# Kernel tuning notes

Measured on AMD Instinct MI355X. Metric: run time of the kernel, lower is better.

The kernel has to match this reference:

```python
import jax, jax.numpy as jnp
import numpy as np

N1 = 100000  # source cloud size (x1)
N2 = 100000  # target cloud size (x2)
F = 64       # point feature dim
E = 1600000  # number of radius edges (avg 16 neighbors)
H = 128      # MLP hidden/out dim


def setup_inputs() -> dict:
    key = jax.random.key(0)
    ks = jax.random.split(key, 12)
    s = 0.05
    return {
        "x1_features": jax.random.normal(ks[0], (N1, F), jnp.float32),
        "x1_pos": jax.random.normal(ks[1], (N1, 3), jnp.float32),
        "x2_features": jax.random.normal(ks[2], (N2, F), jnp.float32),
        "x2_pos": jax.random.normal(ks[3], (N2, 3), jnp.float32),
        "W1": jax.random.normal(ks[4], (2 * F + 3, H), jnp.float32) * s,
        "b1": jnp.zeros((H,), jnp.float32),
        "W2": jax.random.normal(ks[5], (H, H), jnp.float32) * s,
        "b2": jnp.zeros((H,), jnp.float32),
        "W3": jax.random.normal(ks[6], (H, H), jnp.float32) * s,
        "b3": jnp.zeros((H,), jnp.float32),
        "edge_src": jax.random.randint(ks[7], (E,), 0, N1, jnp.int32),
        "edge_dst": jax.random.randint(ks[8], (E,), 0, N2, jnp.int32),
    }


def reference(x1_features, x1_pos, x2_features, x2_pos,
              W1, b1, W2, b2, W3, b3, edge_src, edge_dst):
    # message(x_i, x_j, pos_i, pos_j): i = target (x2, edge_dst), j = source (x1, edge_src)
    # msg = cat([x_i, x_j, pos_j - pos_i], dim=1)  -> [E, 2F+3]
    msg = jnp.concatenate(
        [x2_features[edge_dst],
         x1_features[edge_src],
         x1_pos[edge_src] - x2_pos[edge_dst]], axis=1)
    # MLP (Linear+ReLU x3, FastFlow3D make_mlp style)
    h = jax.nn.relu(msg @ W1 + b1)
    h = jax.nn.relu(h @ W2 + b2)
    h = jax.nn.relu(h @ W3 + b3)
    # scatter-max aggregation onto x2 nodes; PyG fills empty segments with 0
    out = jax.ops.segment_max(h, edge_dst, num_segments=N2)
    out = jnp.where(jnp.isneginf(out), 0.0, out)
    return out, x2_pos
```

## Files before the change

### kernel.cpp

```cpp
#include <hip/hip_runtime.h>
#include <hip/hip_bf16.h>

#define DEV __device__ __forceinline__

typedef short bf16x8 __attribute__((ext_vector_type(8)));
typedef float f32x16 __attribute__((ext_vector_type(16)));

static constexpr int FDIM  = 64;
static constexpr int HH    = 128;
static constexpr int KPAD  = 144;
static constexpr int KS    = KPAD / 16;
static constexpr int TM    = 256;

static constexpr int CSTR  = TM * 16 + 256 + 16;
static constexpr int HBUF  = 16 * CSTR;
static constexpr int L_TOT = HBUF + TM * 4;

static constexpr int WTL      = KPAD * HH;
static constexpr int WT_TOTAL = 3 * WTL;

DEV unsigned pack2(float a, float b) {
    union { __hip_bfloat162 h; unsigned u; } cv;
    cv.h.x = __float2bfloat16(a);
    cv.h.y = __float2bfloat16(b);
    return cv.u;
}
DEV unsigned short f2bf(float f) {
    union { __hip_bfloat16 h; unsigned short u; } cv;
    cv.h = __float2bfloat16(f);
    return cv.u;
}
DEV int rowoff(int r) { return r * 16 + (r >> 3) * 8; }

__global__ void k_cvt(const float* __restrict__ src, unsigned short* __restrict__ dst, int n8) {
    int i = blockIdx.x * 256 + threadIdx.x;
    if (i < n8) {
        float4 a = *(const float4*)(src + (size_t)i * 8);
        float4 b = *(const float4*)(src + (size_t)i * 8 + 4);
        uint4 o;
        o.x = pack2(a.x, a.y); o.y = pack2(a.z, a.w);
        o.z = pack2(b.x, b.y); o.w = pack2(b.z, b.w);
        *(uint4*)(dst + (size_t)i * 8) = o;
    }
}

__global__ void k_wprep(const float* __restrict__ W1, const float* __restrict__ b1,
                        const float* __restrict__ W2, const float* __restrict__ b2,
                        const float* __restrict__ W3, const float* __restrict__ b3,
                        unsigned short* __restrict__ wt) {
    int i = blockIdx.x * 256 + threadIdx.x;
    if (i >= WT_TOTAL) return;
    int layer = i / WTL, j = i % WTL;
    int n = j / KPAD, k = j % KPAD;
    float v = 0.f;
    if (layer == 0) {
        if (k < 131) v = W1[k * HH + n];
        else if (k == 131) v = b1[n];
    } else {
        const float* W = (layer == 1) ? W2 : W3;
        const float* b = (layer == 1) ? b2 : b3;
        if (k < 128) v = W[k * HH + n];
        else if (k == 128) v = b[n];
    }
    wt[i] = f2bf(v);
}

__global__ void k_hist(const int* __restrict__ edst, int* __restrict__ cnt, int E) {
    int e = blockIdx.x * 256 + threadIdx.x;
    if (e < E) atomicAdd(&cnt[edst[e]], 1);
}

__global__ void k_scan_part(const int* __restrict__ cnt, int* __restrict__ partial, int n2) {
    __shared__ int sm[256];
    int t = threadIdx.x;
    int base = blockIdx.x * 1024 + t * 4;
    int s = 0;
#pragma unroll
    for (int j = 0; j < 4; j++) { int idx = base + j; if (idx < n2) s += cnt[idx]; }
    sm[t] = s; __syncthreads();
    for (int off = 128; off > 0; off >>= 1) {
        if (t < off) sm[t] += sm[t + off];
        __syncthreads();
    }
    if (t == 0) partial[blockIdx.x] = sm[0];
}

__global__ void k_scan_top(int* __restrict__ partial, int nb) {
    __shared__ int sm[256];
    int t = threadIdx.x;
    int v = (t < nb) ? partial[t] : 0;
    sm[t] = v; __syncthreads();
    for (int off = 1; off < 256; off <<= 1) {
        int add = (t >= off) ? sm[t - off] : 0;
        __syncthreads();
        sm[t] += add;
        __syncthreads();
    }
    if (t < nb) partial[t] = sm[t] - v;
}

__global__ void k_scan_down(const int* __restrict__ cnt, const int* __restrict__ partial,
                            int* __restrict__ cursor, int n2) {
    __shared__ int sm[256];
    int t = threadIdx.x;
    int base = blockIdx.x * 1024 + t * 4;
    int c[4]; int s = 0;
#pragma unroll
    for (int j = 0; j < 4; j++) { int idx = base + j; c[j] = (idx < n2) ? cnt[idx] : 0; s += c[j]; }
    sm[t] = s; __syncthreads();
    for (int off = 1; off < 256; off <<= 1) {
        int add = (t >= off) ? sm[t - off] : 0;
        __syncthreads();
        sm[t] += add;
        __syncthreads();
    }
    int run = partial[blockIdx.x] + (sm[t] - s);
#pragma unroll
    for (int j = 0; j < 4; j++) {
        int idx = base + j;
        if (idx < n2) cursor[idx] = run;
        run += c[j];
    }
}

__global__ void k_fill(const int* __restrict__ edst, const int* __restrict__ esrc,
                       int* __restrict__ cursor,
                       int* __restrict__ csr_s, int* __restrict__ csr_d, int E) {
    int e = blockIdx.x * 256 + threadIdx.x;
    if (e < E) {
        int d = edst[e];
        int p = atomicAdd(&cursor[d], 1);
        csr_s[p] = esrc[e];
        csr_d[p] = d;
    }
}

DEV f32x16 zerov() {
    f32x16 v;
#pragma unroll
    for (int i = 0; i < 16; i++) v[i] = 0.f;
    return v;
}
DEV float relu(float x) { return fmaxf(x, 0.f); }

DEV void layer_reg(const unsigned short* __restrict__ wtl, const unsigned pkin[32],
                   unsigned pkout[32], int l31, int hh, unsigned biasw) {
    unsigned xv[16];
#pragma unroll
    for (int ks = 0; ks < 8; ks++) {
        unsigned t0 = hh ? pkin[4 * ks + 0] : pkin[4 * ks + 2];
        unsigned t1 = hh ? pkin[4 * ks + 1] : pkin[4 * ks + 3];
        xv[2 * ks + 0] = (unsigned)__shfl_xor((int)t0, 32, 64);
        xv[2 * ks + 1] = (unsigned)__shfl_xor((int)t1, 32, 64);
    }
#pragma unroll
    for (int rt = 0; rt < 4; rt++) {
        f32x16 acc = zerov();
#pragma unroll
        for (int ks = 0; ks < 8; ks++) {
            union { unsigned u[4]; bf16x8 v; } B;
            B.u[0] = hh ? xv[2 * ks + 0]   : pkin[4 * ks + 0];
            B.u[1] = hh ? xv[2 * ks + 1]   : pkin[4 * ks + 1];
            B.u[2] = hh ? pkin[4 * ks + 2] : xv[2 * ks + 0];
            B.u[3] = hh ? pkin[4 * ks + 3] : xv[2 * ks + 1];
            bf16x8 A = *(const bf16x8*)(wtl + (rt * 32 + l31) * KPAD + ks * 16 + 8 * hh);
            acc = __builtin_amdgcn_mfma_f32_32x32x16_bf16(A, B.v, acc, 0, 0, 0);
        }
        {
            union { unsigned u[4]; bf16x8 v; } B;
            B.u[0] = biasw; B.u[1] = 0u; B.u[2] = 0u; B.u[3] = 0u;
            bf16x8 A = *(const bf16x8*)(wtl + (rt * 32 + l31) * KPAD + 8 * 16 + 8 * hh);
            acc = __builtin_amdgcn_mfma_f32_32x32x16_bf16(A, B.v, acc, 0, 0, 0);
        }
#pragma unroll
        for (int g = 0; g < 4; g++) {
            pkout[8 * rt + 2 * g + 0] = pack2(relu(acc[4 * g + 0]), relu(acc[4 * g + 1]));
            pkout[8 * rt + 2 * g + 1] = pack2(relu(acc[4 * g + 2]), relu(acc[4 * g + 3]));
        }
    }
}

template <bool SORTED, bool BF16SRC>
__global__ __launch_bounds__(512, 4) void k_main(
    const float* __restrict__ x1f, const float* __restrict__ x1p,
    const float* __restrict__ x2f, const float* __restrict__ x2p,
    const char* __restrict__ xb1, const char* __restrict__ xb2,
    const unsigned short* __restrict__ wt,
    const int* __restrict__ csr_s, const int* __restrict__ csr_d,
    const int* __restrict__ edge_src, const int* __restrict__ edge_dst,
    float* __restrict__ out, int E) {
    __shared__ __align__(16) char smem[L_TOT];
    char* hbf = smem;
    int*  dl  = (int*)(smem + HBUF);

    const int tid  = threadIdx.x;
    const int lane = tid & 63;
    const int wv   = tid >> 6;
    const int l31  = lane & 31;
    const int hh   = lane >> 5;
    const int eb   = blockIdx.x * TM;
    const int r    = wv * 32 + l31;
    const int slot = eb + r;
    const bool ok  = slot < E;

    int d = 0, s = 0;
    if (ok) {
        d = SORTED ? csr_d[slot] : edge_dst[slot];
        s = SORTED ? csr_s[slot] : edge_src[slot];
    }
    if (hh == 0) dl[r] = ok ? d : -1;

    bf16x8 Bv[KS];
    if (BF16SRC) {
        const char* bx2 = xb2 + (size_t)d * (2 * FDIM);
        const char* bx1 = xb1 + (size_t)s * (2 * FDIM);
#pragma unroll
        for (int ks = 0; ks < 4; ks++)
            Bv[ks] = *(const bf16x8*)(bx2 + (2 * ks + hh) * 16);
#pragma unroll
        for (int ks = 4; ks < 8; ks++)
            Bv[ks] = *(const bf16x8*)(bx1 + (2 * (ks - 4) + hh) * 16);
    } else {
        const float* fx2 = x2f + (size_t)d * FDIM;
        const float* fx1 = x1f + (size_t)s * FDIM;
#pragma unroll
        for (int ks = 0; ks < 8; ks++) {
            const float* b = (ks < 4) ? (fx2 + (2 * ks + hh) * 8)
                                      : (fx1 + (2 * (ks - 4) + hh) * 8);
            float4 a0 = *(const float4*)(b);
            float4 a1 = *(const float4*)(b + 4);
            union { unsigned u[4]; bf16x8 v; } B;
            B.u[0] = pack2(a0.x, a0.y); B.u[1] = pack2(a0.z, a0.w);
            B.u[2] = pack2(a1.x, a1.y); B.u[3] = pack2(a1.z, a1.w);
            Bv[ks] = B.v;
        }
    }
    {
        float dx = 0.f, dy = 0.f, dz = 0.f;
        if (ok) {
            dx = x1p[s * 3 + 0] - x2p[d * 3 + 0];
            dy = x1p[s * 3 + 1] - x2p[d * 3 + 1];
            dz = x1p[s * 3 + 2] - x2p[d * 3 + 2];
        }
        union { unsigned u[4]; bf16x8 v; } P;
        P.u[0] = hh ? 0u : pack2(dx, dy);
        P.u[1] = hh ? 0u : pack2(dz, 1.0f);
        P.u[2] = 0u; P.u[3] = 0u;
        Bv[8] = P.v;
    }

    unsigned pkA[32], pkB[32];
#pragma unroll
    for (int rt = 0; rt < 4; rt++) {
        f32x16 acc = zerov();
#pragma unroll
        for (int ks = 0; ks < KS; ks++) {
            bf16x8 A = *(const bf16x8*)(wt + (rt * 32 + l31) * KPAD + ks * 16 + 8 * hh);
            acc = __builtin_amdgcn_mfma_f32_32x32x16_bf16(A, Bv[ks], acc, 0, 0, 0);
        }
#pragma unroll
        for (int g = 0; g < 4; g++) {
            pkA[8 * rt + 2 * g + 0] = pack2(relu(acc[4 * g + 0]), relu(acc[4 * g + 1]));
            pkA[8 * rt + 2 * g + 1] = pack2(relu(acc[4 * g + 2]), relu(acc[4 * g + 3]));
        }
    }

    const unsigned biasw = hh ? 0u : 0x00003F80u;
    layer_reg(wt + WTL,     pkA, pkB, l31, hh, biasw);
    layer_reg(wt + 2 * WTL, pkB, pkA, l31, hh, biasw);

    {
        char* dst = hbf + rowoff(r) + 8 * hh;
#pragma unroll
        for (int u = 0; u < 16; u++) {
            uint2 w; w.x = pkA[2 * u + 0]; w.y = pkA[2 * u + 1];
            *(uint2*)(dst + u * CSTR) = w;
        }
    }
    __syncthreads();

    {
        const int p     = tid & 63;
        const int strip = tid >> 6;
        const int r0 = strip * 32;
        const char* fbase = hbf + (p >> 2) * CSTR + (p & 3) * 4;
        int curd = dl[r0];
        int rs = r0;
        float m0 = 0.f, m1 = 0.f;
#pragma unroll 4
        for (int rr = r0; rr < r0 + 32; rr++) {
            int dd = dl[rr];
            if (dd != curd) {
                if (curd >= 0) {
                    bool extL = (rs == r0) && (r0 == 0 || dl[r0 - 1] == curd);
                    if (extL) {
                        if (m0 > 0.f) atomicMax((int*)out + (size_t)curd * HH + 2 * p,     __float_as_int(m0));
                        if (m1 > 0.f) atomicMax((int*)out + (size_t)curd * HH + 2 * p + 1, __float_as_int(m1));
                    } else {
                        out[(size_t)curd * HH + 2 * p]     = m0;
                        out[(size_t)curd * HH + 2 * p + 1] = m1;
                    }
                }
                curd = dd; rs = rr; m0 = 0.f; m1 = 0.f;
            }
            unsigned w = *(const unsigned*)(fbase + rowoff(rr));
            m0 = fmaxf(m0, __uint_as_float(w << 16));
            m1 = fmaxf(m1, __uint_as_float(w & 0xffff0000u));
        }
        if (curd >= 0) {
            bool extL = (rs == r0) && (r0 == 0 || dl[r0 - 1] == curd);
            bool extR = (r0 + 32 == TM) || (dl[r0 + 32] == curd);
            if (extL || extR) {
                if (m0 > 0.f) atomicMax((int*)out + (size_t)curd * HH + 2 * p,     __float_as_int(m0));
                if (m1 > 0.f) atomicMax((int*)out + (size_t)curd * HH + 2 * p + 1, __float_as_int(m1));
            } else {
                out[(size_t)curd * HH + 2 * p]     = m0;
                out[(size_t)curd * HH + 2 * p + 1] = m1;
            }
        }
    }
}

extern "C" void kernel_launch(void* const* d_in, const int* in_sizes, int n_in,
                              void* d_out, int out_size, void* d_ws, size_t ws_size,
                              hipStream_t stream) {
    const float* x1f = (const float*)d_in[0];
    const float* x1p = (const float*)d_in[1];
    const float* x2f = (const float*)d_in[2];
    const float* x2p = (const float*)d_in[3];
    const float* W1  = (const float*)d_in[4];
    const float* b1  = (const float*)d_in[5];
    const float* W2  = (const float*)d_in[6];
    const float* b2  = (const float*)d_in[7];
    const float* W3  = (const float*)d_in[8];
    const float* b3  = (const float*)d_in[9];
    const int* esrc  = (const int*)d_in[10];
    const int* edst  = (const int*)d_in[11];
    const int E  = in_sizes[10];
    const int N1 = in_sizes[1] / 3;
    const int N2 = in_sizes[3] / 3;
    float* out = (float*)d_out;

    size_t off = 0;
    auto take = [&](size_t bytes) { size_t o = off; off = (off + bytes + 255) & ~(size_t)255; return o; };
    size_t o_cnt = take(4 * (size_t)N2);
    size_t o_cur = take(4 * (size_t)N2);
    size_t o_par = take(4 * 256);
    size_t o_cs  = take(4 * (size_t)E);
    size_t o_cd  = take(4 * (size_t)E);
    size_t o_wt  = take(2 * (size_t)WT_TOTAL);
    size_t need_csr = off;
    size_t o_x1  = take(2 * (size_t)N1 * FDIM);
    size_t o_x2  = take(2 * (size_t)N2 * FDIM);
    size_t need_bf = off;

    const int NB = (N2 + 1023) / 1024;
    bool use_csr = (need_csr <= ws_size) && (NB <= 256);
    bool use_bf  = (need_bf <= ws_size);

    char* ws = (char*)d_ws;
    unsigned short* wt = use_csr ? (unsigned short*)(ws + o_wt) : (unsigned short*)ws;
    int* cnt    = (int*)(ws + o_cnt);
    int* cursor = (int*)(ws + o_cur);
    int* part   = (int*)(ws + o_par);
    int* csr_s  = (int*)(ws + o_cs);
    int* csr_d  = (int*)(ws + o_cd);
    char* xb1   = ws + o_x1;
    char* xb2   = ws + o_x2;

    (void)hipMemsetAsync(out, 0, (size_t)N2 * HH * 4, stream);
    (void)hipMemcpyAsync(out + (size_t)N2 * HH, x2p, (size_t)N2 * 3 * 4,
                         hipMemcpyDeviceToDevice, stream);

    k_wprep<<<(WT_TOTAL + 255) / 256, 256, 0, stream>>>(W1, b1, W2, b2, W3, b3, wt);

    if (use_bf) {
        int n8_1 = N1 * FDIM / 8, n8_2 = N2 * FDIM / 8;
        k_cvt<<<(n8_1 + 255) / 256, 256, 0, stream>>>(x1f, (unsigned short*)xb1, n8_1);
        k_cvt<<<(n8_2 + 255) / 256, 256, 0, stream>>>(x2f, (unsigned short*)xb2, n8_2);
    }

    const int grid = (E + TM - 1) / TM;
    if (use_csr) {
        (void)hipMemsetAsync(cnt, 0, 4 * (size_t)N2, stream);
        k_hist<<<(E + 255) / 256, 256, 0, stream>>>(edst, cnt, E);
        k_scan_part<<<NB, 256, 0, stream>>>(cnt, part, N2);
        k_scan_top<<<1, 256, 0, stream>>>(part, NB);
        k_scan_down<<<NB, 256, 0, stream>>>(cnt, part, cursor, N2);
        k_fill<<<(E + 255) / 256, 256, 0, stream>>>(edst, esrc, cursor, csr_s, csr_d, E);
        if (use_bf)
            k_main<true, true><<<grid, 512, 0, stream>>>(
                x1f, x1p, x2f, x2p, xb1, xb2, wt, csr_s, csr_d, esrc, edst, out, E);
        else
            k_main<true, false><<<grid, 512, 0, stream>>>(
                x1f, x1p, x2f, x2p, xb1, xb2, wt, csr_s, csr_d, esrc, edst, out, E);
    } else {
        if (use_bf)
            k_main<false, true><<<grid, 512, 0, stream>>>(
                x1f, x1p, x2f, x2p, xb1, xb2, wt, edst, edst, esrc, edst, out, E);
        else
            k_main<false, false><<<grid, 512, 0, stream>>>(
                x1f, x1p, x2f, x2p, xb1, xb2, wt, edst, edst, esrc, edst, out, E);
    }
}
```

Measured before the change: 616.0 us.

## Stage MLP weights in LDS and do segment-max with wave shuffles

All three layers' bf16 weights are re-laid out into per-k-step chunks and copied into a 108KB shared-memory buffer at block start, so MFMA A-operands come from LDS instead of global/L2. The LDS-staged scatter-max is replaced by a segmented shuffle-up scan over each 32-edge half-wave using packed bf16 max, with only segment tails issuing atomicMax. Blocks grow to 1024 threads covering 512 edges. This trades the per-block weight copy and large LDS footprint, which limits blocks per CU, and 32 edge boundaries instead of 256 mean more atomics.

```diff
diff --git a/kernel.cpp b/kernel.cpp
--- a/kernel.cpp
+++ b/kernel.cpp
@@ -5,19 +5,15 @@
 
 typedef short bf16x8 __attribute__((ext_vector_type(8)));
 typedef float f32x16 __attribute__((ext_vector_type(16)));
-
-static constexpr int FDIM  = 64;
-static constexpr int HH    = 128;
-static constexpr int KPAD  = 144;
-static constexpr int KS    = KPAD / 16;
-static constexpr int TM    = 256;
-
-static constexpr int CSTR  = TM * 16 + 256 + 16;
-static constexpr int HBUF  = 16 * CSTR;
-static constexpr int L_TOT = HBUF + TM * 4;
-
-static constexpr int WTL      = KPAD * HH;
-static constexpr int WT_TOTAL = 3 * WTL;
+typedef unsigned short u16x2 __attribute__((ext_vector_type(2)));
+
+static constexpr int FDIM = 64;
+static constexpr int HH   = 128;
+static constexpr int TM   = 512;
+static constexpr int CH   = 4096;
+static constexpr int NCH  = 27;
+static constexpr int WB   = NCH * CH;
+static constexpr int WT_ELEMS = NCH * 2048;
 
 DEV unsigned pack2(float a, float b) {
     union { __hip_bfloat162 h; unsigned u; } cv;
@@ -30,7 +26,11 @@
     cv.h = __float2bfloat16(f);
     return cv.u;
 }
-DEV int rowoff(int r) { return r * 16 + (r >> 3) * 8; }
+DEV unsigned pmax2(unsigned a, unsigned b) {
+    u16x2 av = __builtin_bit_cast(u16x2, a);
+    u16x2 bv = __builtin_bit_cast(u16x2, b);
+    return __builtin_bit_cast(unsigned, __builtin_elementwise_max(av, bv));
+}
 
 __global__ void k_cvt(const float* __restrict__ src, unsigned short* __restrict__ dst, int n8) {
     int i = blockIdx.x * 256 + threadIdx.x;
@@ -49,9 +49,11 @@
                         const float* __restrict__ W3, const float* __restrict__ b3,
                         unsigned short* __restrict__ wt) {
     int i = blockIdx.x * 256 + threadIdx.x;
-    if (i >= WT_TOTAL) return;
-    int layer = i / WTL, j = i % WTL;
-    int n = j / KPAD, k = j % KPAD;
+    if (i >= WT_ELEMS) return;
+    int c = i >> 11, r = i & 2047;
+    int n = r >> 4, half = (r >> 3) & 1, e = r & 7;
+    int layer = c / 9, ks = c % 9;
+    int k = ks * 16 + half * 8 + e;
     float v = 0.f;
     if (layer == 0) {
         if (k < 131) v = W1[k * HH + n];
@@ -143,7 +145,7 @@
 }
 DEV float relu(float x) { return fmaxf(x, 0.f); }
 
-DEV void layer_reg(const unsigned short* __restrict__ wtl, const unsigned pkin[32],
+DEV void layer_reg(const char* __restrict__ wl, const unsigned pkin[32],
                    unsigned pkout[32], int l31, int hh, unsigned biasw) {
     unsigned xv[16];
 #pragma unroll
@@ -155,6 +157,7 @@
     }
 #pragma unroll
     for (int rt = 0; rt < 4; rt++) {
+        const char* arow = wl + (rt * 32 + l31) * 32 + hh * 16;
         f32x16 acc = zerov();
 #pragma unroll
         for (int ks = 0; ks < 8; ks++) {
@@ -163,13 +166,13 @@
             B.u[1] = hh ? xv[2 * ks + 1]   : pkin[4 * ks + 1];
             B.u[2] = hh ? pkin[4 * ks + 2] : xv[2 * ks + 0];
             B.u[3] = hh ? pkin[4 * ks + 3] : xv[2 * ks + 1];
-            bf16x8 A = *(const bf16x8*)(wtl + (rt * 32 + l31) * KPAD + ks * 16 + 8 * hh);
+            bf16x8 A = *(const bf16x8*)(arow + ks * CH);
             acc = __builtin_amdgcn_mfma_f32_32x32x16_bf16(A, B.v, acc, 0, 0, 0);
         }
         {
             union { unsigned u[4]; bf16x8 v; } B;
             B.u[0] = biasw; B.u[1] = 0u; B.u[2] = 0u; B.u[3] = 0u;
-            bf16x8 A = *(const bf16x8*)(wtl + (rt * 32 + l31) * KPAD + 8 * 16 + 8 * hh);
+            bf16x8 A = *(const bf16x8*)(arow + 8 * CH);
             acc = __builtin_amdgcn_mfma_f32_32x32x16_bf16(A, B.v, acc, 0, 0, 0);
         }
 #pragma unroll
@@ -181,7 +184,7 @@
 }
 
 template <bool SORTED, bool BF16SRC>
-__global__ __launch_bounds__(512, 4) void k_main(
+__global__ __launch_bounds__(1024, 4) void k_main(
     const float* __restrict__ x1f, const float* __restrict__ x1p,
     const float* __restrict__ x2f, const float* __restrict__ x2p,
     const char* __restrict__ xb1, const char* __restrict__ xb2,
@@ -189,9 +192,7 @@
     const int* __restrict__ csr_s, const int* __restrict__ csr_d,
     const int* __restrict__ edge_src, const int* __restrict__ edge_dst,
     float* __restrict__ out, int E) {
-    __shared__ __align__(16) char smem[L_TOT];
-    char* hbf = smem;
-    int*  dl  = (int*)(smem + HBUF);
+    __shared__ __align__(16) char wlds[WB];
 
     const int tid  = threadIdx.x;
     const int lane = tid & 63;
@@ -199,21 +200,31 @@
     const int l31  = lane & 31;
     const int hh   = lane >> 5;
     const int eb   = blockIdx.x * TM;
+
+    {
+        const uint4* src = (const uint4*)wt;
+        uint4* dst = (uint4*)wlds;
+#pragma unroll
+        for (int j = tid; j < WB / 16; j += 1024)
+            dst[j] = src[j];
+    }
+    __syncthreads();
+
     const int r    = wv * 32 + l31;
     const int slot = eb + r;
     const bool ok  = slot < E;
-
-    int d = 0, s = 0;
+    int d = -1, s = 0;
     if (ok) {
         d = SORTED ? csr_d[slot] : edge_dst[slot];
         s = SORTED ? csr_s[slot] : edge_src[slot];
     }
-    if (hh == 0) dl[r] = ok ? d : -1;
-
-    bf16x8 Bv[KS];
+    const int dg = (d < 0) ? 0 : d;
+    const int sg = s;
+
+    bf16x8 Bv[9];
     if (BF16SRC) {
-        const char* bx2 = xb2 + (size_t)d * (2 * FDIM);
-        const char* bx1 = xb1 + (size_t)s * (2 * FDIM);
+        const char* bx2 = xb2 + (size_t)dg * (2 * FDIM);
+        const char* bx1 = xb1 + (size_t)sg * (2 * FDIM);
 #pragma unroll
         for (int ks = 0; ks < 4; ks++)
             Bv[ks] = *(const bf16x8*)(bx2 + (2 * ks + hh) * 16);
@@ -221,8 +232,8 @@
         for (int ks = 4; ks < 8; ks++)
             Bv[ks] = *(const bf16x8*)(bx1 + (2 * (ks - 4) + hh) * 16);
     } else {
-        const float* fx2 = x2f + (size_t)d * FDIM;
-        const float* fx1 = x1f + (size_t)s * FDIM;
+        const float* fx2 = x2f + (size_t)dg * FDIM;
+        const float* fx1 = x1f + (size_t)sg * FDIM;
 #pragma unroll
         for (int ks = 0; ks < 8; ks++) {
             const float* b = (ks < 4) ? (fx2 + (2 * ks + hh) * 8)
@@ -238,9 +249,9 @@
     {
         float dx = 0.f, dy = 0.f, dz = 0.f;
         if (ok) {
-            dx = x1p[s * 3 + 0] - x2p[d * 3 + 0];
-            dy = x1p[s * 3 + 1] - x2p[d * 3 + 1];
-            dz = x1p[s * 3 + 2] - x2p[d * 3 + 2];
+            dx = x1p[sg * 3 + 0] - x2p[dg * 3 + 0];
+            dy = x1p[sg * 3 + 1] - x2p[dg * 3 + 1];
+            dz = x1p[sg * 3 + 2] - x2p[dg * 3 + 2];
         }
         union { unsigned u[4]; bf16x8 v; } P;
         P.u[0] = hh ? 0u : pack2(dx, dy);
@@ -252,10 +263,11 @@
     unsigned pkA[32], pkB[32];
 #pragma unroll
     for (int rt = 0; rt < 4; rt++) {
+        const char* arow = wlds + (rt * 32 + l31) * 32 + hh * 16;
         f32x16 acc = zerov();
 #pragma unroll
-        for (int ks = 0; ks < KS; ks++) {
-            bf16x8 A = *(const bf16x8*)(wt + (rt * 32 + l31) * KPAD + ks * 16 + 8 * hh);
+        for (int ks = 0; ks < 9; ks++) {
+            bf16x8 A = *(const bf16x8*)(arow + ks * CH);
             acc = __builtin_amdgcn_mfma_f32_32x32x16_bf16(A, Bv[ks], acc, 0, 0, 0);
         }
 #pragma unroll
@@ -266,57 +278,32 @@
     }
 
     const unsigned biasw = hh ? 0u : 0x00003F80u;
-    layer_reg(wt + WTL,     pkA, pkB, l31, hh, biasw);
-    layer_reg(wt + 2 * WTL, pkB, pkA, l31, hh, biasw);
-
-    {
-        char* dst = hbf + rowoff(r) + 8 * hh;
-#pragma unroll
-        for (int u = 0; u < 16; u++) {
-            uint2 w; w.x = pkA[2 * u + 0]; w.y = pkA[2 * u + 1];
-            *(uint2*)(dst + u * CSTR) = w;
-        }
-    }
-    __syncthreads();
-
-    {
-        const int p     = tid & 63;
-        const int strip = tid >> 6;
-        const int r0 = strip * 32;
-        const char* fbase = hbf + (p >> 2) * CSTR + (p & 3) * 4;
-        int curd = dl[r0];
-        int rs = r0;
-        float m0 = 0.f, m1 = 0.f;
-#pragma unroll 4
-        for (int rr = r0; rr < r0 + 32; rr++) {
-            int dd = dl[rr];
-            if (dd != curd) {
-                if (curd >= 0) {
-                    bool extL = (rs == r0) && (r0 == 0 || dl[r0 - 1] == curd);
-                    if (extL) {
-                        if (m0 > 0.f) atomicMax((int*)out + (size_t)curd * HH + 2 * p,     __float_as_int(m0));
-                        if (m1 > 0.f) atomicMax((int*)out + (size_t)curd * HH + 2 * p + 1, __float_as_int(m1));
-                    } else {
-                        out[(size_t)curd * HH + 2 * p]     = m0;
-                        out[(size_t)curd * HH + 2 * p + 1] = m1;
-                    }
-                }
-                curd = dd; rs = rr; m0 = 0.f; m1 = 0.f;
-            }
-            unsigned w = *(const unsigned*)(fbase + rowoff(rr));
-            m0 = fmaxf(m0, __uint_as_float(w << 16));
-            m1 = fmaxf(m1, __uint_as_float(w & 0xffff0000u));
-        }
-        if (curd >= 0) {
-            bool extL = (rs == r0) && (r0 == 0 || dl[r0 - 1] == curd);
-            bool extR = (r0 + 32 == TM) || (dl[r0 + 32] == curd);
-            if (extL || extR) {
-                if (m0 > 0.f) atomicMax((int*)out + (size_t)curd * HH + 2 * p,     __float_as_int(m0));
-                if (m1 > 0.f) atomicMax((int*)out + (size_t)curd * HH + 2 * p + 1, __float_as_int(m1));
-            } else {
-                out[(size_t)curd * HH + 2 * p]     = m0;
-                out[(size_t)curd * HH + 2 * p + 1] = m1;
-            }
+    layer_reg(wlds + 9 * CH,  pkA, pkB, l31, hh, biasw);
+    layer_reg(wlds + 18 * CH, pkB, pkA, l31, hh, biasw);
+
+    const int dn = __shfl_down(d, 1, 32);
+#pragma unroll
+    for (int off = 1; off < 32; off <<= 1) {
+        int nd = __shfl_up(d, off, 32);
+        bool take = (l31 >= off) && (nd == d);
+#pragma unroll
+        for (int u = 0; u < 32; u++) {
+            unsigned nv = (unsigned)__shfl_up((int)pkA[u], off, 32);
+            unsigned mx = pmax2(pkA[u], nv);
+            pkA[u] = take ? mx : pkA[u];
+        }
+    }
+    const bool flush = (d >= 0) && ((l31 == 31) || (dn != d));
+    if (flush) {
+        int* op = (int*)out + (size_t)d * HH;
+#pragma unroll
+        for (int u = 0; u < 32; u++) {
+            const int feat = 32 * (u >> 3) + 8 * ((u >> 1) & 3) + 4 * hh + 2 * (u & 1);
+            unsigned w = pkA[u];
+            float lo = __uint_as_float(w << 16);
+            float hi = __uint_as_float(w & 0xffff0000u);
+            if (lo > 0.f) atomicMax(op + feat,     __float_as_int(lo));
+            if (hi > 0.f) atomicMax(op + feat + 1, __float_as_int(hi));
         }
     }
 }
@@ -348,7 +335,7 @@
     size_t o_par = take(4 * 256);
     size_t o_cs  = take(4 * (size_t)E);
     size_t o_cd  = take(4 * (size_t)E);
-    size_t o_wt  = take(2 * (size_t)WT_TOTAL);
+    size_t o_wt  = take(2 * (size_t)WT_ELEMS);
     size_t need_csr = off;
     size_t o_x1  = take(2 * (size_t)N1 * FDIM);
     size_t o_x2  = take(2 * (size_t)N2 * FDIM);
@@ -372,7 +359,7 @@
     (void)hipMemcpyAsync(out + (size_t)N2 * HH, x2p, (size_t)N2 * 3 * 4,
                          hipMemcpyDeviceToDevice, stream);
 
-    k_wprep<<<(WT_TOTAL + 255) / 256, 256, 0, stream>>>(W1, b1, W2, b2, W3, b3, wt);
+    k_wprep<<<(WT_ELEMS + 255) / 256, 256, 0, stream>>>(W1, b1, W2, b2, W3, b3, wt);
 
     if (use_bf) {
         int n8_1 = N1 * FDIM / 8, n8_2 = N2 * FDIM / 8;
@@ -389,17 +376,17 @@
         k_scan_down<<<NB, 256, 0, stream>>>(cnt, part, cursor, N2);
         k_fill<<<(E + 255) / 256, 256, 0, stream>>>(edst, esrc, cursor, csr_s, csr_d, E);
         if (use_bf)
-            k_main<true, true><<<grid, 512, 0, stream>>>(
+            k_main<true, true><<<grid, 1024, 0, stream>>>(
                 x1f, x1p, x2f, x2p, xb1, xb2, wt, csr_s, csr_d, esrc, edst, out, E);
         else
-            k_main<true, false><<<grid, 512, 0, stream>>>(
+            k_main<true, false><<<grid, 1024, 0, stream>>>(
                 x1f, x1p, x2f, x2p, xb1, xb2, wt, csr_s, csr_d, esrc, edst, out, E);
     } else {
         if (use_bf)
-            k_main<false, true><<<grid, 512, 0, stream>>>(
+            k_main<false, true><<<grid, 1024, 0, stream>>>(
                 x1f, x1p, x2f, x2p, xb1, xb2, wt, edst, edst, esrc, edst, out, E);
         else
-            k_main<false, false><<<grid, 512, 0, stream>>>(
+            k_main<false, false><<<grid, 1024, 0, stream>>>(
                 x1f, x1p, x2f, x2p, xb1, xb2, wt, edst, edst, esrc, edst, out, E);
     }
 }
```

Result: slower. 664.7 us (+7.9%).
